# Optimization experiments

Hardware: AMD Instinct MI355X
Metric: run time of the kernel (lower is better)

The kernel has to match this reference:

```python
import jax, jax.numpy as jnp
import numpy as np

B, S, E, H, D = 16, 1024, 768, 12, 64  # batch, seq, n_embd, n_head, head_dim
F = 4 * E
EPS = 1e-5


def layernorm(x, g, b):
    mu = jnp.mean(x, axis=-1, keepdims=True)
    var = jnp.mean((x - mu) ** 2, axis=-1, keepdims=True)
    return (x - mu) * jax.lax.rsqrt(var + EPS) * g + b


def setup_inputs() -> dict:
    key = jax.random.key(0)
    ks = jax.random.split(key, 12)
    w = lambda k, shape: jax.random.normal(k, shape, dtype=jnp.float32) * 0.02
    return {
        "x": jax.random.normal(ks[0], (B, S, E), dtype=jnp.float32),
        # per-head q/k/v projections stacked over heads: [H, E, D]
        "Wq": w(ks[1], (H, E, D)), "bq": jnp.zeros((H, D), jnp.float32),
        "Wk": w(ks[2], (H, E, D)), "bk": jnp.zeros((H, D), jnp.float32),
        "Wv": w(ks[3], (H, E, D)), "bv": jnp.zeros((H, D), jnp.float32),
        "Wp": w(ks[4], (E, E)), "bp": jnp.zeros((E,), jnp.float32),
        "ln1_g": jnp.ones((E,), jnp.float32), "ln1_b": jnp.zeros((E,), jnp.float32),
        "ln2_g": jnp.ones((E,), jnp.float32), "ln2_b": jnp.zeros((E,), jnp.float32),
        "W1": w(ks[5], (E, F)), "b1": jnp.zeros((F,), jnp.float32),
        "W2": w(ks[6], (F, E)), "b2": jnp.zeros((E,), jnp.float32),
        "lnf_g": jnp.ones((E,), jnp.float32), "lnf_b": jnp.zeros((E,), jnp.float32),
    }


def reference(x, Wq, bq, Wk, bk, Wv, bv, Wp, bp,
              ln1_g, ln1_b, ln2_g, ln2_b, W1, b1, W2, b2, lnf_g, lnf_b):
    # --- multi-head causal attention (batched over heads, same math as the
    # per-head loop in the original) ---
    h = layernorm(x, ln1_g, ln1_b)
    q = jnp.einsum('bse,hed->bhsd', h, Wq) + bq[None, :, None, :]
    k = jnp.einsum('bse,hed->bhsd', h, Wk) + bk[None, :, None, :]
    v = jnp.einsum('bse,hed->bhsd', h, Wv) + bv[None, :, None, :]
    scores = jnp.einsum('bhsd,bhtd->bhst', q, k)
    causal = jnp.tril(jnp.ones((S, S), dtype=bool))
    # original: mask with -inf, then divide by sqrt(head_dim), then softmax
    scores = jnp.where(causal, scores, -jnp.inf) / np.sqrt(D).astype(np.float32)
    attn = jax.nn.softmax(scores, axis=-1)
    o = jnp.einsum('bhst,bhtd->bhsd', attn, v)
    o = o.transpose(0, 2, 1, 3).reshape(B, S, E)  # concat heads
    x = x + (o @ Wp + bp)
    # --- FFN with post-net LayerNorm (as in the original FeedForward) ---
    h2 = layernorm(x, ln2_g, ln2_b)
    f = jax.nn.gelu(h2 @ W1 + b1, approximate=False) @ W2 + b2
    f = layernorm(f, lnf_g, lnf_b)
    return x + f
```

## Files before the change

### kernel.cpp

```cpp
#include <hip/hip_runtime.h>
#include <math.h>

typedef unsigned short u16;
typedef __attribute__((ext_vector_type(8))) short s16x8;
typedef __attribute__((ext_vector_type(4))) float f32x4;

#define NB 16
#define NS 1024
#define NE 768
#define NH 12
#define ND 64
#define NF 3072
#define NBS (NB*NS)
#define NBH (NB*NH)

__device__ __forceinline__ u16 f2bf(float f){
  unsigned u = __float_as_uint(f);
  unsigned r = (u + 0x7fffu + ((u >> 16) & 1u)) >> 16;
  return (u16)r;
}

__device__ __forceinline__ void gload16(const void* g, void* l){
  __builtin_amdgcn_global_load_lds((const __attribute__((address_space(1))) void*)g,
                                   (__attribute__((address_space(3))) void*)l, 16, 0, 0);
}

__global__ __launch_bounds__(256) void pack_t(const float* __restrict__ W,
                                              u16* __restrict__ Wt, int N, int K){
  __shared__ u16 tile[64*72];
  const int tid = threadIdx.x;
  const int n0 = blockIdx.x*64, k0 = blockIdx.y*64;
  #pragma unroll
  for (int it = 0; it < 4; ++it){
    int c = it*256 + tid;
    int row = c >> 4, col = (c & 15) * 4;
    float4 v = *(const float4*)(W + (size_t)(k0+row)*N + n0 + col);
    tile[row*72+col+0] = f2bf(v.x); tile[row*72+col+1] = f2bf(v.y);
    tile[row*72+col+2] = f2bf(v.z); tile[row*72+col+3] = f2bf(v.w);
  }
  __syncthreads();
  #pragma unroll
  for (int it = 0; it < 2; ++it){
    int c = it*256 + tid;
    int nr = c >> 3, kc = (c & 7) * 8;
    s16x8 val;
    #pragma unroll
    for (int j = 0; j < 8; ++j) val[j] = tile[(kc+j)*72 + nr];
    *(s16x8*)(Wt + (size_t)(n0+nr)*K + k0 + kc) = val;
  }
}

__global__ __launch_bounds__(256) void pack_qkv(const float* __restrict__ Wq,
    const float* __restrict__ Wk, const float* __restrict__ Wv,
    const float* __restrict__ bq, const float* __restrict__ bk,
    const float* __restrict__ bv, u16* __restrict__ Wt, float* __restrict__ bias){
  __shared__ u16 tile[64*72];
  const int tid = threadIdx.x;
  const int n0 = blockIdx.x*64, e0 = blockIdx.y*64;
  const int p = n0 / NE, rr = n0 % NE, h = rr >> 6;
  const float* Wsrc = (p==0) ? Wq : ((p==1) ? Wk : Wv);
  #pragma unroll
  for (int it = 0; it < 4; ++it){
    int c = it*256 + tid;
    int row = c >> 4, col = (c & 15) * 4;
    float4 v = *(const float4*)(Wsrc + ((size_t)h*NE + e0 + row)*ND + col);
    tile[row*72+col+0] = f2bf(v.x); tile[row*72+col+1] = f2bf(v.y);
    tile[row*72+col+2] = f2bf(v.z); tile[row*72+col+3] = f2bf(v.w);
  }
  __syncthreads();
  #pragma unroll
  for (int it = 0; it < 2; ++it){
    int c = it*256 + tid;
    int dr = c >> 3, ec = (c & 7) * 8;
    s16x8 val;
    #pragma unroll
    for (int j = 0; j < 8; ++j) val[j] = tile[(ec+j)*72 + dr];
    *(s16x8*)(Wt + (size_t)(n0+dr)*NE + e0 + ec) = val;
  }
  if (e0 == 0 && tid < 64){
    const float* bsrc = (p==0) ? bq : ((p==1) ? bk : bv);
    bias[n0 + tid] = bsrc[rr + tid];
  }
}

__global__ __launch_bounds__(256) void ln_bf16(const float* __restrict__ x,
    const float* __restrict__ g, const float* __restrict__ b, u16* __restrict__ out){
  __shared__ float red[4];
  const int row = blockIdx.x, tid = threadIdx.x;
  const float* xr = x + (size_t)row*NE;
  float v0 = xr[tid], v1 = xr[tid+256], v2 = xr[tid+512];
  float s = v0 + v1 + v2;
  #pragma unroll
  for (int off = 32; off > 0; off >>= 1) s += __shfl_down(s, off);
  if ((tid & 63) == 0) red[tid >> 6] = s;
  __syncthreads();
  float mu = (red[0]+red[1]+red[2]+red[3]) * (1.f/NE);
  float d0 = v0-mu, d1 = v1-mu, d2 = v2-mu;
  float q = d0*d0 + d1*d1 + d2*d2;
  #pragma unroll
  for (int off = 32; off > 0; off >>= 1) q += __shfl_down(q, off);
  __syncthreads();
  if ((tid & 63) == 0) red[tid >> 6] = q;
  __syncthreads();
  float rs = rsqrtf((red[0]+red[1]+red[2]+red[3]) * (1.f/NE) + 1e-5f);
  u16* orow = out + (size_t)row*NE;
  orow[tid]     = f2bf(d0*rs*g[tid]     + b[tid]);
  orow[tid+256] = f2bf(d1*rs*g[tid+256] + b[tid+256]);
  orow[tid+512] = f2bf(d2*rs*g[tid+512] + b[tid+512]);
}

__global__ __launch_bounds__(256) void ln_add_out(const float* __restrict__ f2,
    const float* __restrict__ g, const float* __restrict__ b, float* __restrict__ x1){
  __shared__ float red[4];
  const int row = blockIdx.x, tid = threadIdx.x;
  const float* xr = f2 + (size_t)row*NE;
  float v0 = xr[tid], v1 = xr[tid+256], v2 = xr[tid+512];
  float s = v0 + v1 + v2;
  #pragma unroll
  for (int off = 32; off > 0; off >>= 1) s += __shfl_down(s, off);
  if ((tid & 63) == 0) red[tid >> 6] = s;
  __syncthreads();
  float mu = (red[0]+red[1]+red[2]+red[3]) * (1.f/NE);
  float d0 = v0-mu, d1 = v1-mu, d2 = v2-mu;
  float q = d0*d0 + d1*d1 + d2*d2;
  #pragma unroll
  for (int off = 32; off > 0; off >>= 1) q += __shfl_down(q, off);
  __syncthreads();
  if ((tid & 63) == 0) red[tid >> 6] = q;
  __syncthreads();
  float rs = rsqrtf((red[0]+red[1]+red[2]+red[3]) * (1.f/NE) + 1e-5f);
  float* orow = x1 + (size_t)row*NE;
  orow[tid]     += d0*rs*g[tid]     + b[tid];
  orow[tid+256] += d1*rs*g[tid+256] + b[tid+256];
  orow[tid+512] += d2*rs*g[tid+512] + b[tid+512];
}

template<int EPI>
__global__ __launch_bounds__(256, 2)
void gemm_bt(const u16* __restrict__ A, const u16* __restrict__ Bt,
             const float* __restrict__ bias, const float* __restrict__ resid,
             float* __restrict__ outF, u16* __restrict__ outU,
             u16* __restrict__ oq, u16* __restrict__ ok, u16* __restrict__ ov,
             int M, int N, int K)
{
  __shared__ u16 As[128*32];
  __shared__ u16 Bs[128*32];
  const int tid = threadIdx.x;
  const int lane = tid & 63, wv = tid >> 6;
  const int wm = wv >> 1, wn = wv & 1;
  const int r = lane & 15, g4 = lane >> 4;
  const int m0 = blockIdx.y*128, n0 = blockIdx.x*128;

  f32x4 acc[4][4] = {};

  for (int kt = 0; kt < K; kt += 32) {
    __syncthreads();
    #pragma unroll
    for (int it = 0; it < 2; ++it) {
      int c = it*256 + tid;
      int row = c >> 2, kc = (c & 3) << 3;
      gload16(A  + (size_t)(m0+row)*K + kt + kc, As + (size_t)(it*256 + wv*64)*8);
      gload16(Bt + (size_t)(n0+row)*K + kt + kc, Bs + (size_t)(it*256 + wv*64)*8);
    }
    __syncthreads();
    s16x8 aF[4], bF[4];
    #pragma unroll
    for (int mi = 0; mi < 4; ++mi)
      aF[mi] = *(const s16x8*)(As + (wm*64 + mi*16 + r)*32 + g4*8);
    #pragma unroll
    for (int ni = 0; ni < 4; ++ni)
      bF[ni] = *(const s16x8*)(Bs + (wn*64 + ni*16 + r)*32 + g4*8);
    #pragma unroll
    for (int mi = 0; mi < 4; ++mi)
      #pragma unroll
      for (int ni = 0; ni < 4; ++ni)
        acc[mi][ni] = __builtin_amdgcn_mfma_f32_16x16x32_bf16(aF[mi], bF[ni], acc[mi][ni], 0, 0, 0);
  }

  const int colb = n0 + wn*64, rowb = m0 + wm*64;
  #pragma unroll
  for (int mi = 0; mi < 4; ++mi) {
    #pragma unroll
    for (int ni = 0; ni < 4; ++ni) {
      const int col = colb + ni*16 + r;
      const float bv = bias[col];
      #pragma unroll
      for (int i = 0; i < 4; ++i) {
        const int row = rowb + mi*16 + g4*4 + i;
        float v = acc[mi][ni][i] + bv;
        if (EPI == 0) {
          int p = col / NE, rr2 = col % NE;
          int hh = rr2 >> 6, d = rr2 & 63;
          int bb = row >> 10, ss = row & (NS-1);
          size_t idx = (((size_t)(bb*NH + hh))*NS + ss)*ND + d;
          if (p == 1) v *= 0.18033688011112042f;
          u16 val = f2bf(v);
          if (p == 0) oq[idx] = val;
          else if (p == 1) ok[idx] = val;
          else ov[idx] = val;
        } else if (EPI == 1) {
          size_t idx = (size_t)row*NE + col;
          outF[idx] = resid[idx] + v;
        } else if (EPI == 2) {
          float ge = 0.5f * v * (1.0f + erff(v * 0.70710678118654752f));
          outU[(size_t)row*NF + col] = f2bf(ge);
        } else {
          outF[(size_t)row*NE + col] = v;
        }
      }
    }
  }
}

__global__ __launch_bounds__(256) void transpose_v(const u16* __restrict__ v,
                                                   u16* __restrict__ vT){
  __shared__ u16 tile[64*80];
  const int tid = threadIdx.x;
  const int t0 = blockIdx.x*64, bh = blockIdx.y;
  const u16* src = v + ((size_t)bh*NS + t0)*ND;
  #pragma unroll
  for (int it = 0; it < 2; ++it){
    int c = it*256 + tid;
    int row = c >> 3, col = (c & 7) * 8;
    *(s16x8*)(tile + row*80 + col) = *(const s16x8*)(src + (size_t)row*ND + col);
  }
  __syncthreads();
  u16* dst = vT + (size_t)bh*ND*NS + t0;
  #pragma unroll
  for (int it = 0; it < 2; ++it){
    int c = it*256 + tid;
    int d = c >> 3, tc = (c & 7) * 8;
    s16x8 val;
    #pragma unroll
    for (int j = 0; j < 8; ++j) val[j] = tile[(tc+j)*80 + d];
    *(s16x8*)(dst + (size_t)d*NS + tc) = val;
  }
}

__global__ __launch_bounds__(256, 2)
void attn(const u16* __restrict__ q, const u16* __restrict__ k,
          const u16* __restrict__ vT, u16* __restrict__ o)
{
  __shared__ u16 Ks[64*80];
  __shared__ u16 Vs[64*80];
  __shared__ u16 Ps[64*80];
  const int tid = threadIdx.x, lane = tid & 63, w = tid >> 6;
  const int r = lane & 15, g4 = lane >> 4;
  const int phys = blockIdx.y * 8 + blockIdx.x;
  const int logical = (phys & 7) * 192 + (phys >> 3);
  const int bh = logical >> 3, qt = logical & 7;
  const int qs0 = qt * 128;
  const int bb = bh / NH, hh = bh % NH;

  s16x8 qf[2][2];
  {
    const u16* qb = q + ((size_t)bh*NS + qs0 + w*16 + r)*ND;
    qf[0][0] = *(const s16x8*)(qb + g4*8);
    qf[0][1] = *(const s16x8*)(qb + 32 + g4*8);
    qf[1][0] = *(const s16x8*)(qb + (size_t)64*ND + g4*8);
    qf[1][1] = *(const s16x8*)(qb + (size_t)64*ND + 32 + g4*8);
  }

  f32x4 oacc[2][4] = {};
  float mrow[2][4], lrow[2][4];
  #pragma unroll
  for (int rg = 0; rg < 2; ++rg)
    #pragma unroll
    for (int i = 0; i < 4; ++i){ mrow[rg][i] = -INFINITY; lrow[rg][i] = 0.f; }

  const u16* kbase = k  + (size_t)bh*NS*ND;
  const u16* vbase = vT + (size_t)bh*ND*NS;
  const int nt = qs0/64 + 2;

  for (int t = 0; t < nt; ++t) {
    const int kt0 = t*64;
    __syncthreads();
    #pragma unroll
    for (int it = 0; it < 2; ++it) {
      int c = it*256 + tid;
      int rowi = c >> 3, coli = (c & 7) * 8;
      *(s16x8*)(Ks + rowi*80 + coli) = *(const s16x8*)(kbase + (size_t)(kt0+rowi)*ND + coli);
      *(s16x8*)(Vs + rowi*80 + coli) = *(const s16x8*)(vbase + (size_t)rowi*NS + kt0 + coli);
    }
    __syncthreads();

    #pragma unroll
    for (int rg = 0; rg < 2; ++rg) {
      const int rgb = qs0 + rg*64;
      if (kt0 > rgb) continue;

      f32x4 sc[4];
      __builtin_amdgcn_s_setprio(1);
      #pragma unroll
      for (int ni = 0; ni < 4; ++ni) {
        s16x8 kf0 = *(const s16x8*)(Ks + (ni*16+r)*80 + g4*8);
        s16x8 kf1 = *(const s16x8*)(Ks + (ni*16+r)*80 + 32 + g4*8);
        f32x4 tacc = {};
        tacc = __builtin_amdgcn_mfma_f32_16x16x32_bf16(qf[rg][0], kf0, tacc, 0, 0, 0);
        tacc = __builtin_amdgcn_mfma_f32_16x16x32_bf16(qf[rg][1], kf1, tacc, 0, 0, 0);
        sc[ni] = tacc;
      }
      __builtin_amdgcn_s_setprio(0);

      float mx[4];
      #pragma unroll
      for (int i = 0; i < 4; ++i) mx[i] = mrow[rg][i];
      if (kt0 == rgb) {
        #pragma unroll
        for (int ni = 0; ni < 4; ++ni)
          #pragma unroll
          for (int i = 0; i < 4; ++i) {
            if (ni*16 + r > w*16 + g4*4 + i) sc[ni][i] = -INFINITY;
            mx[i] = fmaxf(mx[i], sc[ni][i]);
          }
      } else {
        #pragma unroll
        for (int ni = 0; ni < 4; ++ni)
          #pragma unroll
          for (int i = 0; i < 4; ++i) mx[i] = fmaxf(mx[i], sc[ni][i]);
      }
      #pragma unroll
      for (int i = 0; i < 4; ++i) {
        #pragma unroll
        for (int off = 1; off < 16; off <<= 1) mx[i] = fmaxf(mx[i], __shfl_xor(mx[i], off));
      }
      float corr[4], psum[4];
      #pragma unroll
      for (int i = 0; i < 4; ++i) {
        corr[i] = exp2f(mrow[rg][i] - mx[i]);
        mrow[rg][i] = mx[i];
        psum[i] = 0.f;
      }
      #pragma unroll
      for (int ni = 0; ni < 4; ++ni)
        #pragma unroll
        for (int i = 0; i < 4; ++i) {
          float p = exp2f(sc[ni][i] - mrow[rg][i]);
          psum[i] += p;
          Ps[(w*16 + g4*4 + i)*80 + ni*16 + r] = f2bf(p);
        }
      #pragma unroll
      for (int i = 0; i < 4; ++i) {
        #pragma unroll
        for (int off = 1; off < 16; off <<= 1) psum[i] += __shfl_xor(psum[i], off);
        lrow[rg][i] = lrow[rg][i]*corr[i] + psum[i];
      }
      #pragma unroll
      for (int di = 0; di < 4; ++di)
        #pragma unroll
        for (int i = 0; i < 4; ++i) oacc[rg][di][i] *= corr[i];
      __builtin_amdgcn_s_setprio(1);
      #pragma unroll
      for (int kk = 0; kk < 2; ++kk) {
        s16x8 pf = *(const s16x8*)(Ps + (w*16 + r)*80 + kk*32 + g4*8);
        #pragma unroll
        for (int di = 0; di < 4; ++di) {
          s16x8 vf = *(const s16x8*)(Vs + (di*16+r)*80 + kk*32 + g4*8);
          oacc[rg][di] = __builtin_amdgcn_mfma_f32_16x16x32_bf16(pf, vf, oacc[rg][di], 0, 0, 0);
        }
      }
      __builtin_amdgcn_s_setprio(0);
    }
  }

  #pragma unroll
  for (int rg = 0; rg < 2; ++rg)
    #pragma unroll
    for (int i = 0; i < 4; ++i) {
      float inv = 1.f / lrow[rg][i];
      int s = qs0 + rg*64 + w*16 + g4*4 + i;
      u16* orow = o + ((size_t)(bb*NS + s))*NE + hh*ND;
      #pragma unroll
      for (int di = 0; di < 4; ++di)
        orow[di*16 + r] = f2bf(oacc[rg][di][i] * inv);
    }
}

extern "C" void kernel_launch(void* const* d_in, const int* in_sizes, int n_in,
                              void* d_out, int out_size, void* d_ws, size_t ws_size,
                              hipStream_t stream)
{
  const float* x   = (const float*)d_in[0];
  const float* Wq  = (const float*)d_in[1];
  const float* bq  = (const float*)d_in[2];
  const float* Wk  = (const float*)d_in[3];
  const float* bk  = (const float*)d_in[4];
  const float* Wv  = (const float*)d_in[5];
  const float* bv  = (const float*)d_in[6];
  const float* Wp  = (const float*)d_in[7];
  const float* bp  = (const float*)d_in[8];
  const float* g1  = (const float*)d_in[9];
  const float* b1n = (const float*)d_in[10];
  const float* g2  = (const float*)d_in[11];
  const float* b2n = (const float*)d_in[12];
  const float* W1  = (const float*)d_in[13];
  const float* b1f = (const float*)d_in[14];
  const float* W2  = (const float*)d_in[15];
  const float* b2f = (const float*)d_in[16];
  const float* gf  = (const float*)d_in[17];
  const float* bf  = (const float*)d_in[18];

  char* ws = (char*)d_ws;
  u16*   WqkvT = (u16*)(ws + 0);
  u16*   WpT   = (u16*)(ws + 3538944);
  u16*   W1T   = (u16*)(ws + 4718592);
  u16*   W2T   = (u16*)(ws + 9437184);
  float* qkvb  = (float*)(ws + 14155776);
  u16*   hbuf  = (u16*)(ws + 14164992);
  u16*   qbuf  = (u16*)(ws + 39330816);
  u16*   kbuf  = (u16*)(ws + 64496640);
  u16*   vbuf  = (u16*)(ws + 89662464);
  u16*   vTbuf = (u16*)(ws + 114828288);
  const size_t base_end = 139994112;
  float* f2    = (float*)kbuf;
  float* x1    = (float*)d_out;

  const size_t f1_full = (size_t)NBS * NF * 2;
  u16* f1buf;
  int mc;
  if (ws_size >= base_end + f1_full) {
    f1buf = (u16*)(ws + base_end);
    mc = NBS;
  } else {
    f1buf = vbuf;
    size_t cap = (ws_size < base_end ? ws_size : base_end) - 89662464;
    mc = (int)(cap / ((size_t)NF * 2)) / 128 * 128;
    if (mc <= 0) mc = 128;
    if (mc > NBS) mc = NBS;
  }

  pack_qkv<<<dim3(36, 12), 256, 0, stream>>>(Wq, Wk, Wv, bq, bk, bv, WqkvT, qkvb);
  pack_t  <<<dim3(NE/64, NE/64), 256, 0, stream>>>(Wp, WpT, NE, NE);
  pack_t  <<<dim3(NF/64, NE/64), 256, 0, stream>>>(W1, W1T, NF, NE);
  pack_t  <<<dim3(NE/64, NF/64), 256, 0, stream>>>(W2, W2T, NE, NF);

  ln_bf16<<<NBS, 256, 0, stream>>>(x, g1, b1n, hbuf);
  gemm_bt<0><<<dim3(2304/128, NBS/128), 256, 0, stream>>>(hbuf, WqkvT, qkvb, nullptr,
      nullptr, nullptr, qbuf, kbuf, vbuf, NBS, 2304, NE);
  transpose_v<<<dim3(NS/64, NBH), 256, 0, stream>>>(vbuf, vTbuf);
  attn<<<dim3(NS/128, NBH), 256, 0, stream>>>(qbuf, kbuf, vTbuf, hbuf);
  gemm_bt<1><<<dim3(NE/128, NBS/128), 256, 0, stream>>>(hbuf, WpT, bp, x,
      x1, nullptr, nullptr, nullptr, nullptr, NBS, NE, NE);
  ln_bf16<<<NBS, 256, 0, stream>>>(x1, g2, b2n, qbuf);
  for (int r0 = 0; r0 < NBS; r0 += mc) {
    int m = (NBS - r0 < mc) ? (NBS - r0) : mc;
    gemm_bt<2><<<dim3(NF/128, m/128), 256, 0, stream>>>(qbuf + (size_t)r0*NE, W1T, b1f,
        nullptr, nullptr, f1buf, nullptr, nullptr, nullptr, m, NF, NE);
    gemm_bt<3><<<dim3(NE/128, m/128), 256, 0, stream>>>(f1buf, W2T, b2f, nullptr,
        f2 + (size_t)r0*NE, nullptr, nullptr, nullptr, nullptr, m, NE, NF);
  }
  ln_add_out<<<NBS, 256, 0, stream>>>(f2, gf, bf, x1);
}
```

Baseline: 707.5 us.

## Pair causal query tiles for balanced attention work and skip rescaling lazily

Each attention block now handles two 64-row query tiles taken from opposite ends of the sequence (qt and 15-qt), so every block iterates over the same number of key tiles and the causal workload is balanced across blocks. Online softmax rescaling is also made lazy: the running max and the correction of the output and sum accumulators are updated only when some row's max grows by more than a threshold, checked across the whole wave. This cuts exponentials and multiplies on most iterations. It relies on the bounded exponent growth staying within fp32 and bf16 range for the probabilities.

```diff
diff --git a/kernel.cpp b/kernel.cpp
--- a/kernel.cpp
+++ b/kernel.cpp
@@ -249,16 +249,16 @@
   const int phys = blockIdx.y * 8 + blockIdx.x;
   const int logical = (phys & 7) * 192 + (phys >> 3);
   const int bh = logical >> 3, qt = logical & 7;
-  const int qs0 = qt * 128;
   const int bb = bh / NH, hh = bh % NH;
+  const int rgb0 = qt * 64, rgb1 = (15 - qt) * 64;
 
   s16x8 qf[2][2];
   {
-    const u16* qb = q + ((size_t)bh*NS + qs0 + w*16 + r)*ND;
-    qf[0][0] = *(const s16x8*)(qb + g4*8);
-    qf[0][1] = *(const s16x8*)(qb + 32 + g4*8);
-    qf[1][0] = *(const s16x8*)(qb + (size_t)64*ND + g4*8);
-    qf[1][1] = *(const s16x8*)(qb + (size_t)64*ND + 32 + g4*8);
+    const u16* qb = q + ((size_t)bh*NS + w*16 + r)*ND;
+    qf[0][0] = *(const s16x8*)(qb + (size_t)rgb0*ND + g4*8);
+    qf[0][1] = *(const s16x8*)(qb + (size_t)rgb0*ND + 32 + g4*8);
+    qf[1][0] = *(const s16x8*)(qb + (size_t)rgb1*ND + g4*8);
+    qf[1][1] = *(const s16x8*)(qb + (size_t)rgb1*ND + 32 + g4*8);
   }
 
   f32x4 oacc[2][4] = {};
@@ -270,7 +270,7 @@
 
   const u16* kbase = k  + (size_t)bh*NS*ND;
   const u16* vbase = vT + (size_t)bh*ND*NS;
-  const int nt = qs0/64 + 2;
+  const int nt = 16 - qt;
 
   for (int t = 0; t < nt; ++t) {
     const int kt0 = t*64;
@@ -286,7 +286,7 @@
 
     #pragma unroll
     for (int rg = 0; rg < 2; ++rg) {
-      const int rgb = qs0 + rg*64;
+      const int rgb = (rg == 0) ? rgb0 : rgb1;
       if (kt0 > rgb) continue;
 
       f32x4 sc[4];
@@ -324,38 +324,41 @@
         #pragma unroll
         for (int off = 1; off < 16; off <<= 1) mx[i] = fmaxf(mx[i], __shfl_xor(mx[i], off));
       }
-      float corr[4], psum[4];
-      #pragma unroll
-      for (int i = 0; i < 4; ++i) {
-        corr[i] = exp2f(mrow[rg][i] - mx[i]);
-        mrow[rg][i] = mx[i];
-        psum[i] = 0.f;
+      bool nogrow = true;
+      #pragma unroll
+      for (int i = 0; i < 4; ++i) nogrow = nogrow && (mx[i] - mrow[rg][i] <= 8.f);
+      float psum[4];
+      if (!__all(nogrow)) {
+        #pragma unroll
+        for (int i = 0; i < 4; ++i) {
+          float corr = exp2f(mrow[rg][i] - mx[i]);
+          mrow[rg][i] = mx[i];
+          lrow[rg][i] *= corr;
+          #pragma unroll
+          for (int di = 0; di < 4; ++di) oacc[rg][di][i] *= corr;
+        }
       }
       #pragma unroll
       for (int ni = 0; ni < 4; ++ni)
         #pragma unroll
         for (int i = 0; i < 4; ++i) {
           float p = exp2f(sc[ni][i] - mrow[rg][i]);
-          psum[i] += p;
+          if (ni == 0) psum[i] = p; else psum[i] += p;
           Ps[(w*16 + g4*4 + i)*80 + ni*16 + r] = f2bf(p);
         }
       #pragma unroll
       for (int i = 0; i < 4; ++i) {
         #pragma unroll
         for (int off = 1; off < 16; off <<= 1) psum[i] += __shfl_xor(psum[i], off);
-        lrow[rg][i] = lrow[rg][i]*corr[i] + psum[i];
-      }
-      #pragma unroll
-      for (int di = 0; di < 4; ++di)
-        #pragma unroll
-        for (int i = 0; i < 4; ++i) oacc[rg][di][i] *= corr[i];
+        lrow[rg][i] += psum[i];
+      }
       __builtin_amdgcn_s_setprio(1);
       #pragma unroll
       for (int kk = 0; kk < 2; ++kk) {
-        s16x8 pf = *(const s16x8*)(Ps + (w*16 + r)*80 + kk*32 + g4*8);
+        s16x8 pf = *(const s16x8*)(&Ps[(w*16 + r)*80 + kk*32 + g4*8]);
         #pragma unroll
         for (int di = 0; di < 4; ++di) {
-          s16x8 vf = *(const s16x8*)(Vs + (di*16+r)*80 + kk*32 + g4*8);
+          s16x8 vf = *(const s16x8*)(&Vs[(di*16+r)*80 + kk*32 + g4*8]);
           oacc[rg][di] = __builtin_amdgcn_mfma_f32_16x16x32_bf16(pf, vf, oacc[rg][di], 0, 0, 0);
         }
       }
@@ -364,16 +367,18 @@
   }
 
   #pragma unroll
-  for (int rg = 0; rg < 2; ++rg)
+  for (int rg = 0; rg < 2; ++rg) {
+    const int rgb = (rg == 0) ? rgb0 : rgb1;
     #pragma unroll
     for (int i = 0; i < 4; ++i) {
       float inv = 1.f / lrow[rg][i];
-      int s = qs0 + rg*64 + w*16 + g4*4 + i;
+      int s = rgb + w*16 + g4*4 + i;
       u16* orow = o + ((size_t)(bb*NS + s))*NE + hh*ND;
       #pragma unroll
       for (int di = 0; di < 4; ++di)
         orow[di*16 + r] = f2bf(oacc[rg][di][i] * inv);
     }
+  }
 }
 
 extern "C" void kernel_launch(void* const* d_in, const int* in_sizes, int n_in,
@@ -438,7 +443,7 @@
   gemm_bt<0><<<dim3(2304/128, NBS/128), 256, 0, stream>>>(hbuf, WqkvT, qkvb, nullptr,
       nullptr, nullptr, qbuf, kbuf, vbuf, NBS, 2304, NE);
   transpose_v<<<dim3(NS/64, NBH), 256, 0, stream>>>(vbuf, vTbuf);
-  attn<<<dim3(NS/128, NBH), 256, 0, stream>>>(qbuf, kbuf, vTbuf, hbuf);
+  attn<<<dim3(8, NBH), 256, 0, stream>>>(qbuf, kbuf, vTbuf, hbuf);
   gemm_bt<1><<<dim3(NE/128, NBS/128), 256, 0, stream>>>(hbuf, WpT, bp, x,
       x1, nullptr, nullptr, nullptr, nullptr, NBS, NE, NE);
   ln_bf16<<<NBS, 256, 0, stream>>>(x1, g2, b2n, qbuf);
```

After: 655.5 us. 1.08x faster.
